# Optimization experiments

Hardware: AMD Instinct MI355X
Metric: run time of the kernel (lower is better)

Reference implementation:

```python
import jax, jax.numpy as jnp
import numpy as np

N_NODES = 50000
N_EDGES = 800000
IN_DIM = 8
EDGE_DIM = 4
HIDDEN = 16
OUT_DIM = 1


def _lin_init(key, fan_in, fan_out):
    kw, kb = jax.random.split(key)
    bound = 1.0 / np.sqrt(fan_in)
    W = jax.random.uniform(kw, (fan_in, fan_out), minval=-bound, maxval=bound, dtype=jnp.float32)
    b = jax.random.uniform(kb, (fan_out,), minval=-bound, maxval=bound, dtype=jnp.float32)
    return W, b


def setup_inputs() -> dict:
    key = jax.random.key(0)
    ks = jax.random.split(key, 16)
    x = jax.random.normal(ks[0], (N_NODES, IN_DIM), dtype=jnp.float32)
    edge_index = jax.random.randint(ks[1], (2, N_EDGES), 0, N_NODES, dtype=jnp.int32)
    edge_attr = jax.random.normal(ks[2], (N_EDGES, EDGE_DIM), dtype=jnp.float32)

    inp = {"x": x, "edge_index": edge_index, "edge_attr": edge_attr}
    in_dims = [IN_DIM, HIDDEN]
    for i in range(2):
        d_in = in_dims[i]
        W1, b1 = _lin_init(ks[3 + 4 * i], EDGE_DIM, HIDDEN)
        W2, b2 = _lin_init(ks[4 + 4 * i], HIDDEN, d_in * HIDDEN)
        root = jax.random.uniform(ks[5 + 4 * i], (d_in, HIDDEN), minval=-1.0 / np.sqrt(d_in), maxval=1.0 / np.sqrt(d_in), dtype=jnp.float32)
        bias = jnp.zeros((HIDDEN,), dtype=jnp.float32)
        inp[f"eW1_{i}"] = W1; inp[f"eb1_{i}"] = b1
        inp[f"eW2_{i}"] = W2; inp[f"eb2_{i}"] = b2
        inp[f"root_{i}"] = root; inp[f"bias_{i}"] = bias
    mW1, mb1 = _lin_init(ks[11], HIDDEN, HIDDEN)
    mW2, mb2 = _lin_init(ks[12], HIDDEN, OUT_DIM)
    inp["mW1"] = mW1; inp["mb1"] = mb1; inp["mW2"] = mW2; inp["mb2"] = mb2
    return inp


def _nnconv(x, src, dst, edge_attr, eW1, eb1, eW2, eb2, root, bias):
    # edge MLP -> per-edge weight matrix [E, d_in, HIDDEN]
    h = jax.nn.silu(edge_attr @ eW1 + eb1)
    Wedge = (h @ eW2 + eb2).reshape(edge_attr.shape[0], x.shape[1], HIDDEN)
    # gather source features, per-edge matmul, scatter-mean to targets
    msg = jnp.einsum('ei,eio->eo', x[src], Wedge)  # [E, HIDDEN]
    agg = jax.ops.segment_sum(msg, dst, num_segments=N_NODES)
    cnt = jax.ops.segment_sum(jnp.ones((msg.shape[0],), dtype=msg.dtype), dst, num_segments=N_NODES)
    agg = agg / jnp.maximum(cnt, 1.0)[:, None]
    return x @ root + agg + bias


def reference(x, edge_index, edge_attr,
              eW1_0, eb1_0, eW2_0, eb2_0, root_0, bias_0,
              eW1_1, eb1_1, eW2_1, eb2_1, root_1, bias_1,
              mW1, mb1, mW2, mb2):
    src, dst = edge_index[0], edge_index[1]
    x = jax.nn.relu(_nnconv(x, src, dst, edge_attr, eW1_0, eb1_0, eW2_0, eb2_0, root_0, bias_0))
    x = jax.nn.relu(_nnconv(x, src, dst, edge_attr, eW1_1, eb1_1, eW2_1, eb2_1, root_1, bias_1))
    out = jax.nn.sigmoid(jax.nn.silu(x @ mW1 + mb1) @ mW2 + mb2)
    return out
```

## Files before the change

### kernel.cpp

```cpp
#include <hip/hip_runtime.h>

#define NN 50000
#define NE 800000

__device__ __forceinline__ float sigm(float v) { return 1.0f / (1.0f + __expf(-v)); }

__global__ void scan_k1(const int* __restrict__ cnt, int n, int* __restrict__ bsum)
{
    __shared__ int s[256];
    int t = threadIdx.x;
    int base = blockIdx.x * 2048 + t * 8;
    int sum = 0;
#pragma unroll
    for (int q = 0; q < 8; ++q) { int idx = base + q; if (idx < n) sum += cnt[idx]; }
    s[t] = sum;
    __syncthreads();
#pragma unroll
    for (int d = 128; d; d >>= 1) { if (t < d) s[t] += s[t + d]; __syncthreads(); }
    if (t == 0) bsum[blockIdx.x] = s[0];
}

__global__ void scan_k2(int* __restrict__ bsum, int nblocks)
{
    __shared__ int s[512];
    int t = threadIdx.x;
    int v = (t < nblocks) ? bsum[t] : 0;
    s[t] = v;
    __syncthreads();
#pragma unroll
    for (int d = 1; d < 512; d <<= 1) {
        int a = (t >= d) ? s[t - d] : 0;
        __syncthreads();
        s[t] += a;
        __syncthreads();
    }
    if (t < nblocks) bsum[t] = s[t] - v;
}

__global__ void scan_k3(const int* __restrict__ cnt, int n,
                        const int* __restrict__ bsum, int* __restrict__ offset)
{
    __shared__ int s[256];
    int t = threadIdx.x;
    int base = blockIdx.x * 2048 + t * 8;
    int v[8]; int sum = 0;
#pragma unroll
    for (int q = 0; q < 8; ++q) {
        int idx = base + q;
        v[q] = (idx < n) ? cnt[idx] : 0;
        sum += v[q];
    }
    s[t] = sum;
    __syncthreads();
#pragma unroll
    for (int d = 1; d < 256; d <<= 1) {
        int a = (t >= d) ? s[t - d] : 0;
        __syncthreads();
        s[t] += a;
        __syncthreads();
    }
    int run = bsum[blockIdx.x] + ((t > 0) ? s[t - 1] : 0);
#pragma unroll
    for (int q = 0; q < 8; ++q) {
        int idx = base + q;
        if (idx <= n) offset[idx] = run;
        run += v[q];
    }
}

__global__ void build_ranks(const int* __restrict__ ei,
                            int* __restrict__ cnt,
                            unsigned short* __restrict__ rank_s,
                            unsigned short* __restrict__ rank_d)
{
    int e = blockIdx.x * 256 + threadIdx.x;
    int s = ei[e], d = ei[NE + e];
    rank_d[e] = (unsigned short)atomicAdd(cnt + d, 1);
    rank_s[e] = (unsigned short)atomicAdd(cnt + NN + s, 1);
}

__global__ void build_perm(const int* __restrict__ ei,
                           const float* __restrict__ ea,
                           const int* __restrict__ off_all,
                           const unsigned short* __restrict__ rank_s,
                           const unsigned short* __restrict__ rank_d,
                           uint2* __restrict__ pack,
                           float* __restrict__ ea_s)
{
    int e = blockIdx.x * 256 + threadIdx.x;
    int s = ei[e], d = ei[NE + e];
    int spos = off_all[NN + s] - NE + (int)rank_s[e];
    int dp   = off_all[d] + (int)rank_d[e];
    pack[spos] = make_uint2((unsigned)s, (unsigned)dp);
    ((float4*)ea_s)[spos] = ((const float4*)ea)[e];
}

template<int DIN>
__global__ __launch_bounds__(256) void edge_fusedG(
        const float* __restrict__ xin,
        const uint2* __restrict__ pack,
        const float* __restrict__ ea_s,
        const float* __restrict__ eW1,
        const float* __restrict__ eb1,
        const float* __restrict__ eW2,
        const float* __restrict__ eb2,
        const int*   __restrict__ off_all,
        float* __restrict__ msgbuf)
{
    constexpr int MROW = 260;
    constexpr int W2B  = DIN * 16 * 20 * 4;
    constexpr int SMB  = 16 * MROW * 4 + 256 * 4;
    constexpr int UNIB = (W2B > SMB) ? W2B : SMB;
    __shared__ __align__(16) char uni[UNIB];
    float* w2L   = (float*)uni;
    float* smemM = (float*)uni;
    int*   sdp   = (int*)(uni + 16 * MROW * 4);
    __shared__ __align__(16) float4 G4[16 * 69];
    __shared__ __align__(16) float4 xbL[16 * 4];
    __shared__ __align__(16) float  xL[16 * DIN];
    __shared__ __align__(16) float  b2L[DIN * 16];
    __shared__ __align__(16) float4 w1t[16];
    __shared__ __align__(16) float  b1s[16];

    int tid = threadIdx.x;
    int nb  = blockIdx.x * 16;
    if (tid < 16) {
        w1t[tid] = make_float4(eW1[tid], eW1[16 + tid], eW1[32 + tid], eW1[48 + tid]);
        b1s[tid] = eb1[tid];
    }
    for (int t = tid; t < 16 * DIN * 16; t += 256) {
        int k = t / (DIN * 16);
        int rem = t - k * DIN * 16;
        int i = rem >> 4, o = rem & 15;
        w2L[(i * 16 + k) * 20 + o] = eW2[t];
    }
    for (int t = tid; t < DIN * 16; t += 256) b2L[t] = eb2[t];
    for (int t = tid; t < 16 * DIN; t += 256) xL[t] = xin[(size_t)nb * DIN + t];
    __syncthreads();

    {
        int nl = tid >> 4, k = tid & 15;
        const float* xrow = xL + nl * DIN;
#pragma unroll
        for (int ob = 0; ob < 4; ++ob) {
            float4 a4 = make_float4(0.f, 0.f, 0.f, 0.f);
#pragma unroll
            for (int i = 0; i < DIN; ++i) {
                const float4 w = *((const float4*)(w2L + (i * 16 + k) * 20) + ob);
                a4.x += xrow[i] * w.x; a4.y += xrow[i] * w.y;
                a4.z += xrow[i] * w.z; a4.w += xrow[i] * w.w;
            }
            G4[nl * 69 + ob * 17 + k] = a4;
        }
        if (k < 4) {
            int ob = k;
            const float4* b2v = (const float4*)b2L;
            float4 a4 = make_float4(0.f, 0.f, 0.f, 0.f);
#pragma unroll
            for (int i = 0; i < DIN; ++i) {
                float4 b = b2v[i * 4 + ob];
                a4.x += xrow[i] * b.x; a4.y += xrow[i] * b.y;
                a4.z += xrow[i] * b.z; a4.w += xrow[i] * b.w;
            }
            xbL[nl * 4 + ob] = a4;
        }
    }
    __syncthreads();

    int eBeg = off_all[NN + nb] - NE;
    int eEnd = off_all[NN + nb + 16] - NE;
    for (int cb = eBeg; cb < eEnd; cb += 256) {
        int pos = cb + tid;
        bool valid = pos < eEnd;
        uint2 pe = valid ? pack[pos] : make_uint2((unsigned)nb, 0u);
        float4 a = valid ? ((const float4*)ea_s)[pos] : make_float4(0.f, 0.f, 0.f, 0.f);

        float h[16];
#pragma unroll
        for (int j = 0; j < 16; ++j) {
            float4 w = w1t[j];
            float p = b1s[j] + a.x * w.x + a.y * w.y + a.z * w.z + a.w * w.w;
            h[j] = p * sigm(p);
        }

        int sl = (int)pe.x - nb;
        float4 acc[4];
#pragma unroll
        for (int ob = 0; ob < 4; ++ob) acc[ob] = xbL[sl * 4 + ob];
#pragma unroll
        for (int k = 0; k < 16; ++k) {
            float hk = h[k];
#pragma unroll
            for (int ob = 0; ob < 4; ++ob) {
                float4 g = G4[sl * 69 + ob * 17 + k];
                acc[ob].x += hk * g.x; acc[ob].y += hk * g.y;
                acc[ob].z += hk * g.z; acc[ob].w += hk * g.w;
            }
        }

        sdp[tid] = valid ? (int)pe.y : -1;
#pragma unroll
        for (int ob = 0; ob < 4; ++ob) {
            smemM[(ob * 4 + 0) * MROW + tid] = acc[ob].x;
            smemM[(ob * 4 + 1) * MROW + tid] = acc[ob].y;
            smemM[(ob * 4 + 2) * MROW + tid] = acc[ob].z;
            smemM[(ob * 4 + 3) * MROW + tid] = acc[ob].w;
        }
        __syncthreads();
#pragma unroll
        for (int r = 0; r < 16; ++r) {
            int le = r * 16 + (tid >> 4);
            int ch = tid & 15;
            int dp = sdp[le];
            float v = smemM[ch * MROW + le];
            if (dp >= 0) msgbuf[(size_t)dp * 16 + ch] = v;
        }
        __syncthreads();
    }
}

__global__ __launch_bounds__(256) void gather_L0(
        const float* __restrict__ xin,
        const float* __restrict__ root,
        const float* __restrict__ bias,
        const int*   __restrict__ off_all,
        const float* __restrict__ msgbuf,
        float* __restrict__ x1)
{
    __shared__ __align__(16) float rootL[8 * 16];
    __shared__ __align__(16) float biasL[16];
    int tid = threadIdx.x;
    if (tid < 128) rootL[tid] = root[tid];
    if (tid < 16) biasL[tid] = bias[tid];
    __syncthreads();

    int ch = tid & 15;
    int n  = blockIdx.x * 16 + (tid >> 4);
    int s0 = off_all[n], e0 = off_all[n + 1];

    float acc = 0.f;
    for (int j = s0; j < e0; ++j)
        acc += msgbuf[(size_t)j * 16 + ch];
    float v = acc / fmaxf((float)(e0 - s0), 1.0f) + biasL[ch];
#pragma unroll
    for (int i = 0; i < 8; ++i)
        v += xin[(size_t)n * 8 + i] * rootL[i * 16 + ch];
    x1[(size_t)n * 16 + ch] = fmaxf(v, 0.f);
}

__global__ __launch_bounds__(256) void gather_final(
        const float* __restrict__ x1,
        const float* __restrict__ root,
        const float* __restrict__ bias,
        const int*   __restrict__ off_all,
        const float* __restrict__ msgbuf,
        const float* __restrict__ mW1,
        const float* __restrict__ mb1,
        const float* __restrict__ mW2,
        const float* __restrict__ mb2,
        float* __restrict__ out)
{
    __shared__ __align__(16) float rootL[256];
    __shared__ __align__(16) float biasL[16];
    __shared__ __align__(16) float w1m[256];
    __shared__ __align__(16) float b1m[16];
    __shared__ __align__(16) float w2m[16];
    __shared__ float b2m;
    int tid = threadIdx.x;
    rootL[tid] = root[tid];
    w1m[tid] = mW1[tid];
    if (tid < 16) { biasL[tid] = bias[tid]; b1m[tid] = mb1[tid]; w2m[tid] = mW2[tid]; }
    if (tid == 0) b2m = mb2[0];
    __syncthreads();

    int ch = tid & 15;
    int n  = blockIdx.x * 16 + (tid >> 4);
    int s0 = off_all[n], e0 = off_all[n + 1];

    float acc = 0.f;
    for (int j = s0; j < e0; ++j)
        acc += msgbuf[(size_t)j * 16 + ch];
    float v = acc / fmaxf((float)(e0 - s0), 1.0f) + biasL[ch];
#pragma unroll
    for (int i = 0; i < 16; ++i)
        v += x1[(size_t)n * 16 + i] * rootL[i * 16 + ch];
    v = fmaxf(v, 0.f);

    float z = b1m[ch];
#pragma unroll
    for (int o = 0; o < 16; ++o) {
        float vo = __shfl(v, o, 16);
        z += vo * w1m[o * 16 + ch];
    }
    float ss = z * sigm(z) * w2m[ch];
#pragma unroll
    for (int off = 8; off; off >>= 1) ss += __shfl_xor(ss, off, 16);
    if (ch == 0) out[n] = sigm(ss + b2m);
}

extern "C" void kernel_launch(void* const* d_in, const int* in_sizes, int n_in,
                              void* d_out, int out_size, void* d_ws, size_t ws_size,
                              hipStream_t stream) {
    const float* x     = (const float*)d_in[0];
    const int*   ei    = (const int*)  d_in[1];
    const float* ea    = (const float*)d_in[2];
    const float* eW1_0 = (const float*)d_in[3];
    const float* eb1_0 = (const float*)d_in[4];
    const float* eW2_0 = (const float*)d_in[5];
    const float* eb2_0 = (const float*)d_in[6];
    const float* root0 = (const float*)d_in[7];
    const float* bias0 = (const float*)d_in[8];
    const float* eW1_1 = (const float*)d_in[9];
    const float* eb1_1 = (const float*)d_in[10];
    const float* eW2_1 = (const float*)d_in[11];
    const float* eb2_1 = (const float*)d_in[12];
    const float* root1 = (const float*)d_in[13];
    const float* bias1 = (const float*)d_in[14];
    const float* mW1   = (const float*)d_in[15];
    const float* mb1   = (const float*)d_in[16];
    const float* mW2   = (const float*)d_in[17];
    const float* mb2   = (const float*)d_in[18];
    float* out = (float*)d_out;

    const int EG = NE / 256;
    const int GG = NN / 16;
    const int SN = 2 * NN;
    const int SB = (SN + 2047) / 2048;

    int* W = (int*)d_ws;
    int*   off_all = W;
    int*   bsum    = W + 100004;
    unsigned short* rank_s = (unsigned short*)(W + 100516);
    unsigned short* rank_d = (unsigned short*)(W + 500516);
    uint2* pack    = (uint2*)(W + 900516);
    float* ea_s    = (float*)(W + 2500516);
    float* x1      = (float*)(W + 5700516);
    float* msgbuf  = (float*)(W + 6500516);
    int*   cnt     = W + 6500516;

    hipMemsetAsync(cnt, 0, SN * sizeof(int), stream);
    build_ranks<<<EG, 256, 0, stream>>>(ei, cnt, rank_s, rank_d);
    scan_k1<<<SB, 256, 0, stream>>>(cnt, SN, bsum);
    scan_k2<<<1, 512, 0, stream>>>(bsum, SB);
    scan_k3<<<SB, 256, 0, stream>>>(cnt, SN, bsum, off_all);
    build_perm<<<EG, 256, 0, stream>>>(ei, ea, off_all, rank_s, rank_d, pack, ea_s);

    edge_fusedG<8><<<GG, 256, 0, stream>>>(x, pack, ea_s, eW1_0, eb1_0,
                                           eW2_0, eb2_0, off_all, msgbuf);
    gather_L0<<<GG, 256, 0, stream>>>(x, root0, bias0, off_all, msgbuf, x1);

    edge_fusedG<16><<<GG, 256, 0, stream>>>(x1, pack, ea_s, eW1_1, eb1_1,
                                            eW2_1, eb2_1, off_all, msgbuf);
    gather_final<<<GG, 256, 0, stream>>>(x1, root1, bias1, off_all, msgbuf,
                                         mW1, mb1, mW2, mb2, out);
}
```

Before: 332.2 us.

## Fuse layer-0 gather into layer-1 edge kernel and use nontemporal perm stores

Merges the layer-0 mean-aggregation and root transform into the layer-1 edge kernel. Each block aggregates msg0 for its 16 source nodes, keeps x1 in shared memory, and runs the per-edge messages straight away, which removes one kernel launch and the x1 re-read. This works because the node-block to source-edge mapping matches between stages. Messages now use separate buffers (msg0, msg1) because blocks in the fused kernel write msg1 while other blocks may still read msg0. build_perm also writes pack and ea_s with nontemporal stores to reduce cache pollution.

New measurement: 373.4 us. 1.12x slower.

```diff
diff --git a/kernel.cpp b/kernel.cpp
--- a/kernel.cpp
+++ b/kernel.cpp
@@ -4,6 +4,8 @@
 #define NE 800000
 
 __device__ __forceinline__ float sigm(float v) { return 1.0f / (1.0f + __expf(-v)); }
+
+using vfloat4 = float __attribute__((ext_vector_type(4)));
 
 __global__ void scan_k1(const int* __restrict__ cnt, int n, int* __restrict__ bsum)
 {
@@ -84,19 +86,20 @@
                            const int* __restrict__ off_all,
                            const unsigned short* __restrict__ rank_s,
                            const unsigned short* __restrict__ rank_d,
-                           uint2* __restrict__ pack,
+                           unsigned long long* __restrict__ pack,
                            float* __restrict__ ea_s)
 {
     int e = blockIdx.x * 256 + threadIdx.x;
     int s = ei[e], d = ei[NE + e];
     int spos = off_all[NN + s] - NE + (int)rank_s[e];
     int dp   = off_all[d] + (int)rank_d[e];
-    pack[spos] = make_uint2((unsigned)s, (unsigned)dp);
-    ((float4*)ea_s)[spos] = ((const float4*)ea)[e];
-}
-
-template<int DIN>
-__global__ __launch_bounds__(256) void edge_fusedG(
+    unsigned long long pk = (unsigned)s | ((unsigned long long)(unsigned)dp << 32);
+    __builtin_nontemporal_store(pk, pack + spos);
+    vfloat4 av = *(const vfloat4*)(ea + (size_t)e * 4);
+    __builtin_nontemporal_store(av, (vfloat4*)(ea_s + (size_t)spos * 4));
+}
+
+__global__ __launch_bounds__(256) void edge_fusedG8(
         const float* __restrict__ xin,
         const uint2* __restrict__ pack,
         const float* __restrict__ ea_s,
@@ -107,6 +110,7 @@
         const int*   __restrict__ off_all,
         float* __restrict__ msgbuf)
 {
+    constexpr int DIN = 8;
     constexpr int MROW = 260;
     constexpr int W2B  = DIN * 16 * 20 * 4;
     constexpr int SMB  = 16 * MROW * 4 + 256 * 4;
@@ -182,7 +186,6 @@
             float p = b1s[j] + a.x * w.x + a.y * w.y + a.z * w.z + a.w * w.w;
             h[j] = p * sigm(p);
         }
-
         int sl = (int)pe.x - nb;
         float4 acc[4];
 #pragma unroll
@@ -197,7 +200,6 @@
                 acc[ob].z += hk * g.z; acc[ob].w += hk * g.w;
             }
         }
-
         sdp[tid] = valid ? (int)pe.y : -1;
 #pragma unroll
         for (int ob = 0; ob < 4; ++ob) {
@@ -219,33 +221,151 @@
     }
 }
 
-__global__ __launch_bounds__(256) void gather_L0(
+__global__ __launch_bounds__(256) void gather_edge16(
         const float* __restrict__ xin,
-        const float* __restrict__ root,
-        const float* __restrict__ bias,
+        const float* __restrict__ root0,
+        const float* __restrict__ bias0,
+        const float* __restrict__ msg0,
+        const uint2* __restrict__ pack,
+        const float* __restrict__ ea_s,
+        const float* __restrict__ eW1,
+        const float* __restrict__ eb1,
+        const float* __restrict__ eW2,
+        const float* __restrict__ eb2,
         const int*   __restrict__ off_all,
-        const float* __restrict__ msgbuf,
-        float* __restrict__ x1)
-{
-    __shared__ __align__(16) float rootL[8 * 16];
-    __shared__ __align__(16) float biasL[16];
+        float* __restrict__ x1,
+        float* __restrict__ msg1)
+{
+    constexpr int DIN = 16;
+    constexpr int MROW = 260;
+    constexpr int W2B  = DIN * 16 * 20 * 4;
+    constexpr int SMB  = 16 * MROW * 4 + 256 * 4;
+    constexpr int UNIB = (W2B > SMB) ? W2B : SMB;
+    __shared__ __align__(16) char uni[UNIB];
+    float* w2L   = (float*)uni;
+    float* smemM = (float*)uni;
+    int*   sdp   = (int*)(uni + 16 * MROW * 4);
+    __shared__ __align__(16) float4 G4[16 * 69];
+    __shared__ __align__(16) float4 xbL[16 * 4];
+    __shared__ __align__(16) float  x1L[16 * 16];
+    __shared__ __align__(16) float  b2L[DIN * 16];
+    __shared__ __align__(16) float4 w1t[16];
+    __shared__ __align__(16) float  b1s[16];
+    __shared__ __align__(16) float  rootL[8 * 16];
+    __shared__ __align__(16) float  biasL[16];
+
     int tid = threadIdx.x;
-    if (tid < 128) rootL[tid] = root[tid];
-    if (tid < 16) biasL[tid] = bias[tid];
-    __syncthreads();
-
-    int ch = tid & 15;
-    int n  = blockIdx.x * 16 + (tid >> 4);
-    int s0 = off_all[n], e0 = off_all[n + 1];
-
-    float acc = 0.f;
-    for (int j = s0; j < e0; ++j)
-        acc += msgbuf[(size_t)j * 16 + ch];
-    float v = acc / fmaxf((float)(e0 - s0), 1.0f) + biasL[ch];
-#pragma unroll
-    for (int i = 0; i < 8; ++i)
-        v += xin[(size_t)n * 8 + i] * rootL[i * 16 + ch];
-    x1[(size_t)n * 16 + ch] = fmaxf(v, 0.f);
+    int nb  = blockIdx.x * 16;
+    if (tid < 16) {
+        w1t[tid] = make_float4(eW1[tid], eW1[16 + tid], eW1[32 + tid], eW1[48 + tid]);
+        b1s[tid] = eb1[tid];
+        biasL[tid] = bias0[tid];
+    }
+    if (tid < 128) rootL[tid] = root0[tid];
+    for (int t = tid; t < 16 * DIN * 16; t += 256) {
+        int k = t / (DIN * 16);
+        int rem = t - k * DIN * 16;
+        int i = rem >> 4, o = rem & 15;
+        w2L[(i * 16 + k) * 20 + o] = eW2[t];
+    }
+    for (int t = tid; t < DIN * 16; t += 256) b2L[t] = eb2[t];
+    __syncthreads();
+
+    {
+        int ch = tid & 15;
+        int nl = tid >> 4;
+        int n  = nb + nl;
+        int s0 = off_all[n], e0 = off_all[n + 1];
+        float acc = 0.f;
+        for (int j = s0; j < e0; ++j)
+            acc += msg0[(size_t)j * 16 + ch];
+        float v = acc / fmaxf((float)(e0 - s0), 1.0f) + biasL[ch];
+#pragma unroll
+        for (int i = 0; i < 8; ++i)
+            v += xin[(size_t)n * 8 + i] * rootL[i * 16 + ch];
+        v = fmaxf(v, 0.f);
+        x1[(size_t)n * 16 + ch] = v;
+        x1L[nl * 16 + ch] = v;
+    }
+    __syncthreads();
+
+    {
+        int nl = tid >> 4, k = tid & 15;
+        const float* xrow = x1L + nl * DIN;
+#pragma unroll
+        for (int ob = 0; ob < 4; ++ob) {
+            float4 a4 = make_float4(0.f, 0.f, 0.f, 0.f);
+#pragma unroll
+            for (int i = 0; i < DIN; ++i) {
+                const float4 w = *((const float4*)(w2L + (i * 16 + k) * 20) + ob);
+                a4.x += xrow[i] * w.x; a4.y += xrow[i] * w.y;
+                a4.z += xrow[i] * w.z; a4.w += xrow[i] * w.w;
+            }
+            G4[nl * 69 + ob * 17 + k] = a4;
+        }
+        if (k < 4) {
+            int ob = k;
+            const float4* b2v = (const float4*)b2L;
+            float4 a4 = make_float4(0.f, 0.f, 0.f, 0.f);
+#pragma unroll
+            for (int i = 0; i < DIN; ++i) {
+                float4 b = b2v[i * 4 + ob];
+                a4.x += xrow[i] * b.x; a4.y += xrow[i] * b.y;
+                a4.z += xrow[i] * b.z; a4.w += xrow[i] * b.w;
+            }
+            xbL[nl * 4 + ob] = a4;
+        }
+    }
+    __syncthreads();
+
+    int eBeg = off_all[NN + nb] - NE;
+    int eEnd = off_all[NN + nb + 16] - NE;
+    for (int cb = eBeg; cb < eEnd; cb += 256) {
+        int pos = cb + tid;
+        bool valid = pos < eEnd;
+        uint2 pe = valid ? pack[pos] : make_uint2((unsigned)nb, 0u);
+        float4 a = valid ? ((const float4*)ea_s)[pos] : make_float4(0.f, 0.f, 0.f, 0.f);
+
+        float h[16];
+#pragma unroll
+        for (int j = 0; j < 16; ++j) {
+            float4 w = w1t[j];
+            float p = b1s[j] + a.x * w.x + a.y * w.y + a.z * w.z + a.w * w.w;
+            h[j] = p * sigm(p);
+        }
+        int sl = (int)pe.x - nb;
+        float4 acc[4];
+#pragma unroll
+        for (int ob = 0; ob < 4; ++ob) acc[ob] = xbL[sl * 4 + ob];
+#pragma unroll
+        for (int k = 0; k < 16; ++k) {
+            float hk = h[k];
+#pragma unroll
+            for (int ob = 0; ob < 4; ++ob) {
+                float4 g = G4[sl * 69 + ob * 17 + k];
+                acc[ob].x += hk * g.x; acc[ob].y += hk * g.y;
+                acc[ob].z += hk * g.z; acc[ob].w += hk * g.w;
+            }
+        }
+        sdp[tid] = valid ? (int)pe.y : -1;
+#pragma unroll
+        for (int ob = 0; ob < 4; ++ob) {
+            smemM[(ob * 4 + 0) * MROW + tid] = acc[ob].x;
+            smemM[(ob * 4 + 1) * MROW + tid] = acc[ob].y;
+            smemM[(ob * 4 + 2) * MROW + tid] = acc[ob].z;
+            smemM[(ob * 4 + 3) * MROW + tid] = acc[ob].w;
+        }
+        __syncthreads();
+#pragma unroll
+        for (int r = 0; r < 16; ++r) {
+            int le = r * 16 + (tid >> 4);
+            int ch = tid & 15;
+            int dp = sdp[le];
+            float v = smemM[ch * MROW + le];
+            if (dp >= 0) msg1[(size_t)dp * 16 + ch] = v;
+        }
+        __syncthreads();
+    }
 }
 
 __global__ __launch_bounds__(256) void gather_final(
@@ -332,10 +452,11 @@
     int*   bsum    = W + 100004;
     unsigned short* rank_s = (unsigned short*)(W + 100516);
     unsigned short* rank_d = (unsigned short*)(W + 500516);
-    uint2* pack    = (uint2*)(W + 900516);
+    unsigned long long* pack = (unsigned long long*)(W + 900516);
     float* ea_s    = (float*)(W + 2500516);
     float* x1      = (float*)(W + 5700516);
-    float* msgbuf  = (float*)(W + 6500516);
+    float* msg0    = (float*)(W + 6500516);
+    float* msg1    = (float*)(W + 19300516);
     int*   cnt     = W + 6500516;
 
     hipMemsetAsync(cnt, 0, SN * sizeof(int), stream);
@@ -345,12 +466,11 @@
     scan_k3<<<SB, 256, 0, stream>>>(cnt, SN, bsum, off_all);
     build_perm<<<EG, 256, 0, stream>>>(ei, ea, off_all, rank_s, rank_d, pack, ea_s);
 
-    edge_fusedG<8><<<GG, 256, 0, stream>>>(x, pack, ea_s, eW1_0, eb1_0,
-                                           eW2_0, eb2_0, off_all, msgbuf);
-    gather_L0<<<GG, 256, 0, stream>>>(x, root0, bias0, off_all, msgbuf, x1);
-
-    edge_fusedG<16><<<GG, 256, 0, stream>>>(x1, pack, ea_s, eW1_1, eb1_1,
-                                            eW2_1, eb2_1, off_all, msgbuf);
-    gather_final<<<GG, 256, 0, stream>>>(x1, root1, bias1, off_all, msgbuf,
+    edge_fusedG8<<<GG, 256, 0, stream>>>(x, (const uint2*)pack, ea_s, eW1_0, eb1_0,
+                                         eW2_0, eb2_0, off_all, msg0);
+    gather_edge16<<<GG, 256, 0, stream>>>(x, root0, bias0, msg0, (const uint2*)pack,
+                                          ea_s, eW1_1, eb1_1, eW2_1, eb2_1,
+                                          off_all, x1, msg1);
+    gather_final<<<GG, 256, 0, stream>>>(x1, root1, bias1, off_all, msg1,
                                          mW1, mb1, mW2, mb2, out);
 }
```
